# Kernel tuning notes

Hardware: AMD Instinct MI355X
Metric: run time of the kernel (lower is better)

The kernel has to match this reference:

```python
import jax, jax.numpy as jnp
import numpy as np

B, S, H, NH = 2, 2048, 1024, 16


def setup_inputs() -> dict:
    key = jax.random.key(0)
    ks = jax.random.split(key, 5)
    x = jax.random.normal(ks[0], (B, S, H), dtype=jnp.float32)
    # causal mask: True = attend
    mask = jnp.tril(jnp.ones((S, S), dtype=bool))[None, None, :, :]
    scale = 1.0 / np.sqrt(H)
    Wq = jax.random.normal(ks[1], (H, H), dtype=jnp.float32) * scale
    Wk = jax.random.normal(ks[2], (H, H), dtype=jnp.float32) * scale
    Wv = jax.random.normal(ks[3], (H, H), dtype=jnp.float32) * scale
    Wo = jax.random.normal(ks[4], (H, H), dtype=jnp.float32) * scale
    return {"x": x, "mask": mask, "Wq": Wq, "Wk": Wk, "Wv": Wv, "Wo": Wo}


def _split_heads(t, n_heads):
    b, s, h = t.shape
    return t.reshape(b, s, n_heads, h // n_heads).transpose(0, 2, 1, 3)  # (b,h,s,d)


def reference(x, mask, Wq, Wk, Wv, Wo):
    q = _split_heads(x @ Wq, NH)
    k = _split_heads(x @ Wk, NH)
    v = _split_heads(x @ Wv, NH)
    d_head = q.shape[-1]
    scores = jnp.einsum('bhqd,bhkd->bhqk', q, k) / jnp.sqrt(jnp.asarray(d_head, q.dtype))
    neg = jnp.asarray(jnp.finfo(scores.dtype).min, scores.dtype)
    scores = jnp.where(mask, scores, neg)  # mask_to_bias: True->0 bias, False->-inf
    attn = jax.nn.softmax(scores, axis=-1)
    out = jnp.einsum('bhqk,bhkd->bhqd', attn, v)
    out = out.transpose(0, 2, 1, 3).reshape(x.shape[0], x.shape[1], -1)  # merge heads
    return out @ Wo
```

## Files before the change

kernel.cpp:

```cpp
#include <hip/hip_runtime.h>

using u16 = unsigned short;
typedef __attribute__((ext_vector_type(8))) __bf16 bf16x8;
typedef __attribute__((ext_vector_type(4))) float f32x4;
typedef __attribute__((ext_vector_type(8))) u16 u16x8;
typedef __attribute__((ext_vector_type(4))) u16 u16x4;
typedef __attribute__((ext_vector_type(4))) float floatx4;

__device__ __forceinline__ u16 f2b(float f) {
    __bf16 h = (__bf16)f;
    return __builtin_bit_cast(u16, h);
}

__device__ __forceinline__ void gload16(const void* g, void* l) {
    __builtin_amdgcn_global_load_lds((const __attribute__((address_space(1))) void*)g,
                                     (__attribute__((address_space(3))) void*)l, 16, 0, 0);
}

constexpr int Hdim = 1024, Bdim = 2, Sdim = 2048, Dh = 64;
constexpr int NTOK = Bdim * Sdim;

__global__ void cast_x_kernel(const float* __restrict__ x, u16* __restrict__ xb, int n4) {
    int i = blockIdx.x * blockDim.x + threadIdx.x;
    int stride = gridDim.x * blockDim.x;
    for (; i < n4; i += stride) {
        floatx4 v = reinterpret_cast<const floatx4*>(x)[i];
        u16x4 o;
        #pragma unroll
        for (int j = 0; j < 4; ++j) o[j] = f2b(v[j]);
        reinterpret_cast<u16x4*>(xb)[i] = o;
    }
}

__global__ void transpose_cast_w(const float* __restrict__ W0, const float* __restrict__ W1,
                                 const float* __restrict__ W2, const float* __restrict__ W3,
                                 u16* __restrict__ T0, u16* __restrict__ T1,
                                 u16* __restrict__ T2, u16* __restrict__ T3) {
    __shared__ float tile[32][33];
    const float* W; u16* T;
    switch (blockIdx.z) {
        case 0: W = W0; T = T0; break;
        case 1: W = W1; T = T1; break;
        case 2: W = W2; T = T2; break;
        default: W = W3; T = T3; break;
    }
    int bx = blockIdx.x * 32, by = blockIdx.y * 32;
    int tx = threadIdx.x, ty = threadIdx.y;
    #pragma unroll
    for (int i = 0; i < 4; ++i)
        tile[ty + i * 8][tx] = W[(size_t)(by + ty + i * 8) * Hdim + bx + tx];
    __syncthreads();
    #pragma unroll
    for (int i = 0; i < 4; ++i)
        T[(size_t)(bx + ty + i * 8) * Hdim + by + tx] = f2b(tile[tx][ty + i * 8]);
}

template <int MODE, int BN>
__global__ __launch_bounds__(256) void gemm_bt(const u16* __restrict__ A, const u16* __restrict__ Bt,
                                               void* __restrict__ C0, void* __restrict__ C1,
                                               void* __restrict__ C2, int N, int K) {
    constexpr int NB = BN / 32;
    __shared__ __align__(16) u16 As[128 * 32];
    __shared__ __align__(16) u16 Bs[BN * 32];
    const int tid = threadIdx.x;
    const int lane = tid & 63, wid = tid >> 6;
    const int wr = wid >> 1, wc = wid & 1;
    const int fr = lane & 15, g = lane >> 4, k8 = g * 8;
    const int rowBase = blockIdx.y * 128, colBase = blockIdx.x * BN;
    const int sr = lane >> 2, sc = (lane & 3) * 8;
    f32x4 acc[4][NB] = {};
    for (int k0 = 0; k0 < K; k0 += 32) {
        __syncthreads();
        #pragma unroll
        for (int i = 0; i < 2; ++i) {
            const int rb = wid * 32 + i * 16;
            gload16(&A[(size_t)(rowBase + rb + sr) * K + k0 + sc], &As[rb * 32]);
        }
        if constexpr (BN == 128) {
            #pragma unroll
            for (int i = 0; i < 2; ++i) {
                const int rb = wid * 32 + i * 16;
                gload16(&Bt[(size_t)(colBase + rb + sr) * K + k0 + sc], &Bs[rb * 32]);
            }
        } else {
            const int rb = wid * 16;
            gload16(&Bt[(size_t)(colBase + rb + sr) * K + k0 + sc], &Bs[rb * 32]);
        }
        __syncthreads();
        bf16x8 af[4], bfr[NB];
        #pragma unroll
        for (int m = 0; m < 4; ++m)
            af[m] = *reinterpret_cast<const bf16x8*>(&As[(wr * 64 + m * 16 + fr) * 32 + k8]);
        #pragma unroll
        for (int n = 0; n < NB; ++n)
            bfr[n] = *reinterpret_cast<const bf16x8*>(&Bs[(wc * (BN / 2) + n * 16 + fr) * 32 + k8]);
        #pragma unroll
        for (int m = 0; m < 4; ++m)
            #pragma unroll
            for (int n = 0; n < NB; ++n)
                acc[m][n] = __builtin_amdgcn_mfma_f32_16x16x32_bf16(af[m], bfr[n], acc[m][n], 0, 0, 0);
    }
    #pragma unroll
    for (int m = 0; m < 4; ++m) {
        #pragma unroll
        for (int n = 0; n < NB; ++n) {
            const int row = rowBase + wr * 64 + m * 16 + g * 4;
            const int col = colBase + wc * (BN / 2) + n * 16 + fr;
            if constexpr (MODE == 0) {
                u16* C = (u16*)C0;
                #pragma unroll
                for (int j = 0; j < 4; ++j) C[(size_t)(row + j) * N + col] = f2b(acc[m][n][j]);
            } else if constexpr (MODE == 1) {
                float* C = (float*)C0;
                #pragma unroll
                for (int j = 0; j < 4; ++j) C[(size_t)(row + j) * N + col] = acc[m][n][j];
            } else {
                if (col < 1024) {
                    u16* Qm = (u16*)C0;
                    #pragma unroll
                    for (int j = 0; j < 4; ++j) Qm[(size_t)(row + j) * 1024 + col] = f2b(acc[m][n][j]);
                } else if (col < 2048) {
                    u16* Km = (u16*)C1;
                    #pragma unroll
                    for (int j = 0; j < 4; ++j) Km[(size_t)(row + j) * 1024 + (col - 1024)] = f2b(acc[m][n][j]);
                } else {
                    u16* Vt = (u16*)C2;
                    u16x4 pk;
                    #pragma unroll
                    for (int j = 0; j < 4; ++j) pk[j] = f2b(acc[m][n][j]);
                    *reinterpret_cast<u16x4*>(&Vt[(size_t)(col - 2048) * NTOK + row]) = pk;
                }
            }
        }
    }
}

__global__ __launch_bounds__(256, 2) void attn_kernel(const u16* __restrict__ Q, const u16* __restrict__ Km,
                                                      const u16* __restrict__ VtG, u16* __restrict__ AO) {
    __shared__ __align__(16) u16 Kt[2][64 * 64];
    __shared__ __align__(16) u16 Vt[2][64 * 64];
    __shared__ __align__(16) u16 Pw[4][32][72];
    const int tid = threadIdx.x, lane = tid & 63, w = tid >> 6;
    const int bid = blockIdx.x;
    const int xg = bid & 7, rem = bid >> 3;
    const int p = rem & 15, yg = rem >> 4;
    const int grp = xg + 8 * yg;
    const int h = grp & 15, b = grp >> 4;
    const int qsel[2] = { p, 31 - p };
    const int h0 = h * Dh;
    const size_t boff = (size_t)b * Sdim * Hdim;
    const u16* Qb = Q + boff;
    u16* AOb = AO + boff;
    const int fr = lane & 15, g = lane >> 4;

    const int lr = lane >> 3;
    const int lc8 = ((lane & 7) ^ lr) * 8;
    const u16* Kg = Km + boff + (size_t)(w * 8 + lr) * Hdim + h0 + lc8;
    const u16* Vg = VtG + (size_t)(h0 + w * 8 + lr) * NTOK + (size_t)b * Sdim + lc8;

    auto stage = [&](int t, int bufi) {
        const int kv0 = t * 64;
        #pragma unroll
        for (int i = 0; i < 2; ++i) {
            gload16(Kg + (size_t)(kv0 + i * 32) * Hdim, &Kt[bufi][w * 512 + i * 2048]);
            gload16(Vg + (size_t)(i * 32) * NTOK + kv0, &Vt[bufi][w * 512 + i * 2048]);
        }
    };

    constexpr float QSCALE = 0.125f * 1.44269504089f;
    bf16x8 qf[2][2];
    int qrow0[2];
    #pragma unroll
    for (int m = 0; m < 2; ++m) {
        qrow0[m] = qsel[m] * 64 + w * 16;
        #pragma unroll
        for (int c = 0; c < 2; ++c) {
            bf16x8 t = *reinterpret_cast<const bf16x8*>(
                &Qb[(size_t)(qrow0[m] + fr) * Hdim + h0 + c * 32 + g * 8]);
            bf16x8 r;
            #pragma unroll
            for (int j = 0; j < 8; ++j) r[j] = (__bf16)((float)t[j] * QSCALE);
            qf[m][c] = r;
        }
    }

    f32x4 o[2][4] = {};
    float mrow[2][4], lrow[2][4];
    #pragma unroll
    for (int m = 0; m < 2; ++m)
        #pragma unroll
        for (int j = 0; j < 4; ++j) { mrow[m][j] = -INFINITY; lrow[m][j] = 0.f; }

    const int ntiles = qsel[1] + 1;
    stage(0, 0);
    __syncthreads();
    int buf = 0;
    for (int t = 0; t < ntiles; ++t) {
        if (t + 1 < ntiles) stage(t + 1, buf ^ 1);
        const int kv0 = t * 64;
        #pragma unroll
        for (int m = 0; m < 2; ++m) {
            if (t > qsel[m]) continue;
            const bool masked = (t == qsel[m]);
            f32x4 s[4];
            __builtin_amdgcn_s_setprio(1);
            #pragma unroll
            for (int n = 0; n < 4; ++n) {
                const int row = n * 16 + fr;
                const int sw = (row & 7) << 3;
                const u16* kp = &Kt[buf][row * 64];
                bf16x8 kf0 = *reinterpret_cast<const bf16x8*>(&kp[(g * 8) ^ sw]);
                bf16x8 kf1 = *reinterpret_cast<const bf16x8*>(&kp[(32 + g * 8) ^ sw]);
                f32x4 z = {};
                z = __builtin_amdgcn_mfma_f32_16x16x32_bf16(qf[m][0], kf0, z, 0, 0, 0);
                s[n] = __builtin_amdgcn_mfma_f32_16x16x32_bf16(qf[m][1], kf1, z, 0, 0, 0);
            }
            __builtin_amdgcn_s_setprio(0);
            #pragma unroll
            for (int j = 0; j < 4; ++j) {
                const int qrow = qrow0[m] + g * 4 + j;
                float mx = -3.0e38f;
                #pragma unroll
                for (int n = 0; n < 4; ++n) {
                    float v = s[n][j];
                    if (masked) {
                        int kv = kv0 + n * 16 + fr;
                        v = (kv <= qrow) ? v : -3.0e38f;
                        s[n][j] = v;
                    }
                    mx = fmaxf(mx, v);
                }
                #pragma unroll
                for (int off = 1; off < 16; off <<= 1) mx = fmaxf(mx, __shfl_xor(mx, off));
                const bool skip = (__all(mx <= mrow[m][j] + 8.0f) != 0);
                const float mnew = skip ? mrow[m][j] : fmaxf(mrow[m][j], mx);
                float rs = 0.f;
                #pragma unroll
                for (int n = 0; n < 4; ++n) {
                    float pv = exp2f(s[n][j] - mnew);
                    rs += pv;
                    Pw[w][m * 16 + g * 4 + j][n * 16 + fr] = f2b(pv);
                }
                #pragma unroll
                for (int off = 1; off < 16; off <<= 1) rs += __shfl_xor(rs, off);
                if (skip) {
                    lrow[m][j] += rs;
                } else {
                    const float alpha = exp2f(mrow[m][j] - mnew);
                    lrow[m][j] = lrow[m][j] * alpha + rs;
                    mrow[m][j] = mnew;
                    #pragma unroll
                    for (int n = 0; n < 4; ++n) o[m][n][j] *= alpha;
                }
            }
            bf16x8 pa0 = *reinterpret_cast<const bf16x8*>(&Pw[w][m * 16 + fr][g * 8]);
            bf16x8 pa1 = *reinterpret_cast<const bf16x8*>(&Pw[w][m * 16 + fr][32 + g * 8]);
            __builtin_amdgcn_s_setprio(1);
            #pragma unroll
            for (int n = 0; n < 4; ++n) {
                const int row = n * 16 + fr;
                const int sw = (row & 7) << 3;
                const u16* vp = &Vt[buf][row * 64];
                bf16x8 vf0 = *reinterpret_cast<const bf16x8*>(&vp[(g * 8) ^ sw]);
                bf16x8 vf1 = *reinterpret_cast<const bf16x8*>(&vp[(32 + g * 8) ^ sw]);
                o[m][n] = __builtin_amdgcn_mfma_f32_16x16x32_bf16(pa0, vf0, o[m][n], 0, 0, 0);
                o[m][n] = __builtin_amdgcn_mfma_f32_16x16x32_bf16(pa1, vf1, o[m][n], 0, 0, 0);
            }
            __builtin_amdgcn_s_setprio(0);
        }
        __syncthreads();
        buf ^= 1;
    }

    #pragma unroll
    for (int m = 0; m < 2; ++m) {
        float invl[4];
        #pragma unroll
        for (int j = 0; j < 4; ++j) invl[j] = 1.0f / lrow[m][j];
        #pragma unroll
        for (int n = 0; n < 4; ++n)
            #pragma unroll
            for (int j = 0; j < 4; ++j) {
                int qrow = qrow0[m] + g * 4 + j;
                AOb[(size_t)qrow * Hdim + h0 + n * 16 + fr] = f2b(o[m][n][j] * invl[j]);
            }
    }
}

extern "C" void kernel_launch(void* const* d_in, const int* in_sizes, int n_in,
                              void* d_out, int out_size, void* d_ws, size_t ws_size,
                              hipStream_t stream) {
    const float* x  = (const float*)d_in[0];
    const float* Wq = (const float*)d_in[2];
    const float* Wk = (const float*)d_in[3];
    const float* Wv = (const float*)d_in[4];
    const float* Wo = (const float*)d_in[5];
    float* out = (float*)d_out;

    u16* ws  = (u16*)d_ws;
    u16* Xb  = ws;
    u16* WqT = ws  + 4194304;
    u16* WkT = WqT + 1048576;
    u16* WvT = WkT + 1048576;
    u16* WoT = WvT + 1048576;
    u16* Qm  = WoT + 1048576;
    u16* Km  = Qm  + 4194304;
    u16* Vt  = Km  + 4194304;
    u16* AO  = Vt  + 4194304;

    cast_x_kernel<<<2048, 256, 0, stream>>>(x, Xb, NTOK * Hdim / 4);
    transpose_cast_w<<<dim3(32, 32, 4), dim3(32, 8), 0, stream>>>(Wq, Wk, Wv, Wo, WqT, WkT, WvT, WoT);
    gemm_bt<2, 128><<<dim3(24, 32), 256, 0, stream>>>(Xb, WqT, Qm, Km, Vt, 3072, Hdim);
    attn_kernel<<<dim3(512), 256, 0, stream>>>(Qm, Km, Vt, AO);
    gemm_bt<1, 64><<<dim3(16, 32), 256, 0, stream>>>(AO, WoT, out, nullptr, nullptr, Hdim, Hdim);
}
```

Baseline: 238.2 us.

## Transpose QK^T MFMA so each lane owns one query row for softmax

The QK^T MFMA operands are swapped so the score fragment is transposed: each lane holds one query row across 16 key columns, which reduces the row max and sum reductions from 4-step 16-lane shuffles per row to two cross-group shuffles. The P tile is written to LDS as packed 4-element stores and the per-wave P buffer shrinks to 16 rows. Online softmax state becomes one scalar per lane, and alpha and 1/l are redistributed to the O accumulator layout with __shfl. This cuts shuffle and LDS-store overhead in the softmax stage, at the cost of extra shuffles when rescaling and a rewritten masking index scheme.

```diff
diff --git a/kernel.cpp b/kernel.cpp
--- a/kernel.cpp
+++ b/kernel.cpp
@@ -139,7 +139,7 @@
                                                       const u16* __restrict__ VtG, u16* __restrict__ AO) {
     __shared__ __align__(16) u16 Kt[2][64 * 64];
     __shared__ __align__(16) u16 Vt[2][64 * 64];
-    __shared__ __align__(16) u16 Pw[4][32][72];
+    __shared__ __align__(16) u16 Pw[4][16][72];
     const int tid = threadIdx.x, lane = tid & 63, w = tid >> 6;
     const int bid = blockIdx.x;
     const int xg = bid & 7, rem = bid >> 3;
@@ -185,11 +185,8 @@
     }
 
     f32x4 o[2][4] = {};
-    float mrow[2][4], lrow[2][4];
-    #pragma unroll
-    for (int m = 0; m < 2; ++m)
-        #pragma unroll
-        for (int j = 0; j < 4; ++j) { mrow[m][j] = -INFINITY; lrow[m][j] = 0.f; }
+    float mrow[2] = { -INFINITY, -INFINITY };
+    float lrow[2] = { 0.f, 0.f };
 
     const int ntiles = qsel[1] + 1;
     stage(0, 0);
@@ -212,49 +209,57 @@
                 bf16x8 kf0 = *reinterpret_cast<const bf16x8*>(&kp[(g * 8) ^ sw]);
                 bf16x8 kf1 = *reinterpret_cast<const bf16x8*>(&kp[(32 + g * 8) ^ sw]);
                 f32x4 z = {};
-                z = __builtin_amdgcn_mfma_f32_16x16x32_bf16(qf[m][0], kf0, z, 0, 0, 0);
-                s[n] = __builtin_amdgcn_mfma_f32_16x16x32_bf16(qf[m][1], kf1, z, 0, 0, 0);
+                z = __builtin_amdgcn_mfma_f32_16x16x32_bf16(kf0, qf[m][0], z, 0, 0, 0);
+                s[n] = __builtin_amdgcn_mfma_f32_16x16x32_bf16(kf1, qf[m][1], z, 0, 0, 0);
             }
             __builtin_amdgcn_s_setprio(0);
-            #pragma unroll
-            for (int j = 0; j < 4; ++j) {
-                const int qrow = qrow0[m] + g * 4 + j;
-                float mx = -3.0e38f;
-                #pragma unroll
-                for (int n = 0; n < 4; ++n) {
-                    float v = s[n][j];
-                    if (masked) {
-                        int kv = kv0 + n * 16 + fr;
-                        v = (kv <= qrow) ? v : -3.0e38f;
-                        s[n][j] = v;
+            if (masked) {
+                const int qr = qrow0[m] + fr;
+                #pragma unroll
+                for (int n = 0; n < 4; ++n)
+                    #pragma unroll
+                    for (int j = 0; j < 4; ++j) {
+                        const int kv = kv0 + n * 16 + g * 4 + j;
+                        if (kv > qr) s[n][j] = -3.0e38f;
                     }
-                    mx = fmaxf(mx, v);
+            }
+            float mx = -3.0e38f;
+            #pragma unroll
+            for (int n = 0; n < 4; ++n)
+                mx = fmaxf(mx, fmaxf(fmaxf(s[n][0], s[n][1]), fmaxf(s[n][2], s[n][3])));
+            mx = fmaxf(mx, __shfl_xor(mx, 16));
+            mx = fmaxf(mx, __shfl_xor(mx, 32));
+            const bool skip = (__all(mx <= mrow[m] + 8.0f) != 0);
+            const float mnew = skip ? mrow[m] : fmaxf(mrow[m], mx);
+            float rs = 0.f;
+            #pragma unroll
+            for (int n = 0; n < 4; ++n) {
+                u16x4 pk;
+                #pragma unroll
+                for (int j = 0; j < 4; ++j) {
+                    const float pv = exp2f(s[n][j] - mnew);
+                    rs += pv;
+                    pk[j] = f2b(pv);
                 }
-                #pragma unroll
-                for (int off = 1; off < 16; off <<= 1) mx = fmaxf(mx, __shfl_xor(mx, off));
-                const bool skip = (__all(mx <= mrow[m][j] + 8.0f) != 0);
-                const float mnew = skip ? mrow[m][j] : fmaxf(mrow[m][j], mx);
-                float rs = 0.f;
-                #pragma unroll
-                for (int n = 0; n < 4; ++n) {
-                    float pv = exp2f(s[n][j] - mnew);
-                    rs += pv;
-                    Pw[w][m * 16 + g * 4 + j][n * 16 + fr] = f2b(pv);
+                *reinterpret_cast<u16x4*>(&Pw[w][fr][n * 16 + g * 4]) = pk;
+            }
+            rs += __shfl_xor(rs, 16);
+            rs += __shfl_xor(rs, 32);
+            if (skip) {
+                lrow[m] += rs;
+            } else {
+                const float alpha = exp2f(mrow[m] - mnew);
+                lrow[m] = lrow[m] * alpha + rs;
+                mrow[m] = mnew;
+                #pragma unroll
+                for (int j = 0; j < 4; ++j) {
+                    const float aj = __shfl(alpha, g * 4 + j);
+                    #pragma unroll
+                    for (int n = 0; n < 4; ++n) o[m][n][j] *= aj;
                 }
-                #pragma unroll
-                for (int off = 1; off < 16; off <<= 1) rs += __shfl_xor(rs, off);
-                if (skip) {
-                    lrow[m][j] += rs;
-                } else {
-                    const float alpha = exp2f(mrow[m][j] - mnew);
-                    lrow[m][j] = lrow[m][j] * alpha + rs;
-                    mrow[m][j] = mnew;
-                    #pragma unroll
-                    for (int n = 0; n < 4; ++n) o[m][n][j] *= alpha;
-                }
-            }
-            bf16x8 pa0 = *reinterpret_cast<const bf16x8*>(&Pw[w][m * 16 + fr][g * 8]);
-            bf16x8 pa1 = *reinterpret_cast<const bf16x8*>(&Pw[w][m * 16 + fr][32 + g * 8]);
+            }
+            bf16x8 pa0 = *reinterpret_cast<const bf16x8*>(&Pw[w][fr][g * 8]);
+            bf16x8 pa1 = *reinterpret_cast<const bf16x8*>(&Pw[w][fr][32 + g * 8]);
             __builtin_amdgcn_s_setprio(1);
             #pragma unroll
             for (int n = 0; n < 4; ++n) {
@@ -274,16 +279,15 @@
 
     #pragma unroll
     for (int m = 0; m < 2; ++m) {
-        float invl[4];
-        #pragma unroll
-        for (int j = 0; j < 4; ++j) invl[j] = 1.0f / lrow[m][j];
-        #pragma unroll
-        for (int n = 0; n < 4; ++n)
-            #pragma unroll
-            for (int j = 0; j < 4; ++j) {
-                int qrow = qrow0[m] + g * 4 + j;
-                AOb[(size_t)qrow * Hdim + h0 + n * 16 + fr] = f2b(o[m][n][j] * invl[j]);
-            }
+        const float invl = 1.0f / lrow[m];
+        #pragma unroll
+        for (int j = 0; j < 4; ++j) {
+            const float ij = __shfl(invl, g * 4 + j);
+            const int qrow = qrow0[m] + g * 4 + j;
+            #pragma unroll
+            for (int n = 0; n < 4; ++n)
+                AOb[(size_t)qrow * Hdim + h0 + n * 16 + fr] = f2b(o[m][n][j] * ij);
+        }
     }
 }
 
```

After: 208.0 us. 1.15x faster.
